# Kernel tuning notes

Measured on AMD Instinct MI355X. Metric: run time of the kernel, lower is better.

The kernel has to match this reference:

```python
import jax, jax.numpy as jnp
import numpy as np

N_NODES = 100000
IN_CH = 128
HID_CH = 128
N_EDGES = 1600000


def setup_inputs() -> dict:
    key = jax.random.key(0)
    ks = jax.random.split(key, 8)
    x = jax.random.normal(ks[0], (N_NODES, IN_CH), dtype=jnp.float32)
    edge_index = jax.random.randint(ks[1], (2, N_EDGES), 0, N_NODES, dtype=jnp.int64)
    s1 = 1.0 / np.sqrt(IN_CH)
    s2 = 1.0 / np.sqrt(HID_CH)
    # SAGEConv layer 1: lin_l (aggregated neighbors, has bias), lin_r (root)
    Wl1 = jax.random.uniform(ks[2], (IN_CH, HID_CH), jnp.float32, -s1, s1)
    Wr1 = jax.random.uniform(ks[3], (IN_CH, HID_CH), jnp.float32, -s1, s1)
    b1 = jnp.zeros((HID_CH,), jnp.float32)
    # SAGEConv layer 2
    Wl2 = jax.random.uniform(ks[4], (HID_CH, HID_CH), jnp.float32, -s2, s2)
    Wr2 = jax.random.uniform(ks[5], (HID_CH, HID_CH), jnp.float32, -s2, s2)
    b2 = jnp.zeros((HID_CH,), jnp.float32)
    return {"x": x, "edge_index": edge_index,
            "Wl1": Wl1, "Wr1": Wr1, "b1": b1,
            "Wl2": Wl2, "Wr2": Wr2, "b2": b2}


def _sage_conv(x, src, dst, inv_deg, Wl, Wr, b):
    # mean aggregation of source-node features into destination nodes
    agg = jax.ops.segment_sum(x[src], dst, num_segments=N_NODES)  # [N, d]
    mean = agg * inv_deg[:, None]
    # out = lin_l(mean_neighbors) + lin_r(x)
    return mean @ Wl + x @ Wr + b


def reference(x, edge_index, Wl1, Wr1, b1, Wl2, Wr2, b2):
    src = edge_index[0]
    dst = edge_index[1]
    deg = jax.ops.segment_sum(jnp.ones_like(dst, dtype=jnp.float32), dst,
                              num_segments=N_NODES)
    inv_deg = 1.0 / jnp.maximum(deg, 1.0)
    h = jax.nn.relu(_sage_conv(x, src, dst, inv_deg, Wl1, Wr1, b1))
    # F.dropout(p=0.2, training=False) is identity in eval mode
    h = jax.nn.relu(_sage_conv(h, src, dst, inv_deg, Wl2, Wr2, b2))
    return h
```

## Files before the change

kernel.cpp:

```cpp
#include <hip/hip_runtime.h>

#define NN 100000
#define NE 1600000
#define CH 128

#define PART 512
#define NP 196
#define PCAP 8704
#define EPB 4096
#define NB 391
#define SCAP 64
#define SLAB 1536

typedef __attribute__((ext_vector_type(8))) short bf16x8;
typedef __attribute__((ext_vector_type(4))) float f32x4;
typedef unsigned int uint;
typedef unsigned short ushort;

__device__ __forceinline__ ushort f2b(float f) {
    uint u = __builtin_bit_cast(uint, f);
    uint r = (u + 0x7fff + ((u >> 16) & 1)) >> 16;
    return (ushort)r;
}
__device__ __forceinline__ float blo(uint v) { return __builtin_bit_cast(float, v << 16); }
__device__ __forceinline__ float bhi(uint v) { return __builtin_bit_cast(float, v & 0xffff0000u); }

__device__ __forceinline__ void acc8(float* a, uint4 v) {
    a[0] += blo(v.x); a[1] += bhi(v.x);
    a[2] += blo(v.y); a[3] += bhi(v.y);
    a[4] += blo(v.z); a[5] += bhi(v.z);
    a[6] += blo(v.w); a[7] += bhi(v.w);
}


__global__ __launch_bounds__(1024) void k_bin(const int4* __restrict__ src4, const int4* __restrict__ dst4,
                                              uint* __restrict__ pcnt, uint* __restrict__ pairbuf) {
    __shared__ uint slots[NP * SCAP];
    __shared__ uint lcnt[NP];
    __shared__ uint lbase[NP];
    int tid = threadIdx.x;
    if (tid < NP) lcnt[tid] = 0;
    __syncthreads();
    int e4 = blockIdx.x * 1024 + tid;
    if (e4 < NE / 4) {
        int4 d4 = dst4[e4];
        int4 s4 = src4[e4];
        int dd[4] = {d4.x, d4.y, d4.z, d4.w};
        int ss[4] = {s4.x, s4.y, s4.z, s4.w};
        #pragma unroll
        for (int j = 0; j < 4; ++j) {
            int p = dd[j] >> 9;
            uint pair = ((uint)(dd[j] & 511) << 17) | (uint)ss[j];
            uint pos = atomicAdd(&lcnt[p], 1u);
            if (pos < SCAP) slots[p * SCAP + pos] = pair;
        }
    }
    __syncthreads();
    if (tid < NP) {
        uint c = lcnt[tid];
        c = c < SCAP ? c : SCAP;
        lcnt[tid] = c;
        lbase[tid] = atomicAdd(&pcnt[tid], c);
    }
    __syncthreads();
    for (int t = tid; t < NP * SCAP; t += 1024) {
        int p = t >> 6;
        uint s = (uint)(t & (SCAP - 1));
        if (s < lcnt[p]) {
            uint idx = lbase[p] + s;
            if (idx < PCAP) pairbuf[(size_t)p * PCAP + idx] = slots[t];
        }
    }
}


__global__ __launch_bounds__(512) void k_csr(const uint* __restrict__ pcnt, const uint* __restrict__ pairbuf,
                                             int* __restrict__ nbrG, uint* __restrict__ pack) {
    __shared__ uint pairs[PCAP];
    __shared__ uint cnt[PART];
    __shared__ uint rowptr[PART + 1];
    __shared__ uint tsum[PART];
    int tid = threadIdx.x;
    int p = blockIdx.x;
    uint tot = pcnt[p];
    tot = tot < PCAP ? tot : PCAP;
    for (uint i = tid; i < tot; i += 512) pairs[i] = pairbuf[(size_t)p * PCAP + i];
    cnt[tid] = 0;
    __syncthreads();
    for (uint i = tid; i < tot; i += 512) atomicAdd(&cnt[pairs[i] >> 17], 1u);
    __syncthreads();
    uint s = cnt[tid];
    tsum[tid] = s;
    __syncthreads();
    for (int off = 1; off < 512; off <<= 1) {
        uint t = (tid >= off) ? tsum[tid - off] : 0;
        __syncthreads();
        tsum[tid] += t;
        __syncthreads();
    }
    rowptr[tid] = tsum[tid] - s;
    if (tid == 511) rowptr[512] = tsum[511];
    __syncthreads();
    cnt[tid] = 0;
    __syncthreads();
    for (uint i = tid; i < tot; i += 512) {
        uint u = pairs[i];
        uint dl = u >> 17;
        uint pos = rowptr[dl] + atomicAdd(&cnt[dl], 1u);
        nbrG[(size_t)p * PCAP + pos] = (int)(u & 0x1FFFFu);
    }
    {
        int n = p * PART + tid;
        if (n < NN) {
            uint deg = rowptr[tid + 1] - rowptr[tid];
            pack[n] = ((uint)(p * PCAP) + rowptr[tid]) | (deg << 21);
        }
    }
}


__global__ __launch_bounds__(256) void k_castx(const float* __restrict__ x, ushort* __restrict__ xb) {
    int n = blockIdx.x * 256 + threadIdx.x;
    int p = blockIdx.y;
    if (n >= NN) return;
    const float4* sp = (const float4*)(x + (size_t)n * 128 + p * 32);
    uint4 o[4];
    ushort* op = (ushort*)o;
    #pragma unroll
    for (int q = 0; q < 8; ++q) {
        float4 v = sp[q];
        op[q * 4 + 0] = f2b(v.x);
        op[q * 4 + 1] = f2b(v.y);
        op[q * 4 + 2] = f2b(v.z);
        op[q * 4 + 3] = f2b(v.w);
    }
    uint4* dp = (uint4*)(xb + ((size_t)p * NN + n) * 32);
    #pragma unroll
    for (int q = 0; q < 4; ++q) dp[q] = o[q];
}

__global__ __launch_bounds__(256) void k_castw(const float* __restrict__ Wl1, const float* __restrict__ Wr1,
                                               const float* __restrict__ Wl2, const float* __restrict__ Wr2,
                                               ushort* __restrict__ BtK1, ushort* __restrict__ BtK2) {
    int i = blockIdx.x * 256 + threadIdx.x;
    const float* Wl = blockIdx.y ? Wl2 : Wl1;
    const float* Wr = blockIdx.y ? Wr2 : Wr1;
    ushort* BtK = blockIdx.y ? BtK2 : BtK1;
    int c = i & 31;
    int n = (i >> 5) & 127;
    int kt = i >> 12;
    int k = kt * 32 + c;
    float v = (k < 128) ? Wl[k * 128 + n] : Wr[(k - 128) * 128 + n];
    BtK[i] = f2b(v);
}


__global__ __launch_bounds__(256) void k_agg(const uint4* __restrict__ feat, const int* __restrict__ nbrG,
                                             const uint* __restrict__ pack, uint4* __restrict__ outb) {
    __shared__ int sl[SLAB];
    __shared__ int sh_s0, sh_cnt;
    int plane = blockIdx.x;
    int nb = blockIdx.y * 64;
    int tid = threadIdx.x;
    int n = nb + (tid >> 2);
    int h = tid & 3;
    if (tid == 0) {
        uint u0 = pack[nb];
        int last = nb + 63 < NN ? nb + 63 : NN - 1;
        uint u1 = pack[last];
        int s0 = (int)(u0 & 0x1FFFFFu);
        sh_s0 = s0;
        sh_cnt = (int)(u1 & 0x1FFFFFu) + (int)(u1 >> 21) - s0;
    }
    __syncthreads();
    int s0 = sh_s0, scnt = sh_cnt;
    bool staged = scnt <= SLAB;
    if (staged) {
        for (int i = tid; i < scnt; i += 256) sl[i] = nbrG[s0 + i];
    }
    __syncthreads();
    if (n >= NN) return;
    uint u = pack[n];
    int s = (int)(u & 0x1FFFFFu);
    int d = (int)(u >> 21);
    const char* fb = (const char*)feat + ((size_t)plane * NN) * 64;
    uint hoff = (uint)h * 16;
    float a[8] = {};
    if (staged) {
        const int* bp = sl + (s - s0);
        int i = 0;
        for (; i + 8 <= d; i += 8) {
            uint off[8];
            uint4 v[8];
            #pragma unroll
            for (int j = 0; j < 8; ++j) off[j] = ((uint)bp[i + j] << 6) | hoff;
            #pragma unroll
            for (int j = 0; j < 8; ++j) v[j] = *(const uint4*)(fb + off[j]);
            #pragma unroll
            for (int j = 0; j < 8; ++j) acc8(a, v[j]);
        }
        for (; i < d; ++i) acc8(a, *(const uint4*)(fb + (((uint)bp[i] << 6) | hoff)));
    } else {
        const int* bp = nbrG + s;
        int i = 0;
        for (; i + 4 <= d; i += 4) {
            uint o0 = ((uint)bp[i] << 6) | hoff;
            uint o1 = ((uint)bp[i + 1] << 6) | hoff;
            uint o2 = ((uint)bp[i + 2] << 6) | hoff;
            uint o3 = ((uint)bp[i + 3] << 6) | hoff;
            uint4 v0 = *(const uint4*)(fb + o0);
            uint4 v1 = *(const uint4*)(fb + o1);
            uint4 v2 = *(const uint4*)(fb + o2);
            uint4 v3 = *(const uint4*)(fb + o3);
            acc8(a, v0);
            acc8(a, v1);
            acc8(a, v2);
            acc8(a, v3);
        }
        for (; i < d; ++i) acc8(a, *(const uint4*)(fb + (((uint)bp[i] << 6) | hoff)));
    }
    float id = 1.0f / fmaxf((float)d, 1.0f);
    uint4 r;
    r.x = (uint)f2b(a[0] * id) | ((uint)f2b(a[1] * id) << 16);
    r.y = (uint)f2b(a[2] * id) | ((uint)f2b(a[3] * id) << 16);
    r.z = (uint)f2b(a[4] * id) | ((uint)f2b(a[5] * id) << 16);
    r.w = (uint)f2b(a[6] * id) | ((uint)f2b(a[7] * id) << 16);
    outb[((size_t)plane * NN + n) * 4 + h] = r;
}


template <bool WB16>
__global__ __launch_bounds__(256) void k_gemm(const ushort* __restrict__ Am, const ushort* Ax,
                                              const ushort* __restrict__ BtK, const float* __restrict__ bias,
                                              void* outp, int M) {
    int lane = threadIdx.x & 63;
    int wave = threadIdx.x >> 6;
    int bm = blockIdx.x * 128 + wave * 32;
    int l16 = lane & 15;
    int lk8 = (lane >> 4) * 8;

    f32x4 acc[2][8] = {};
    #pragma unroll
    for (int kt = 0; kt < 8; ++kt) {
        const ushort* A = (kt < 4) ? Am : Ax;
        int p = kt & 3;
        bf16x8 af[2];
        #pragma unroll
        for (int mt = 0; mt < 2; ++mt) {
            int row = bm + mt * 16 + l16;
            row = row < M ? row : M - 1;
            af[mt] = *(const bf16x8*)(A + ((size_t)p * NN + row) * 32 + lk8);
        }
        const ushort* Bk = BtK + (size_t)kt * 128 * 32;
        #pragma unroll
        for (int nt = 0; nt < 8; ++nt) {
            bf16x8 bfr = *(const bf16x8*)(Bk + (size_t)(nt * 16 + l16) * 32 + lk8);
            acc[0][nt] = __builtin_amdgcn_mfma_f32_16x16x32_bf16(af[0], bfr, acc[0][nt], 0, 0, 0);
            acc[1][nt] = __builtin_amdgcn_mfma_f32_16x16x32_bf16(af[1], bfr, acc[1][nt], 0, 0, 0);
        }
    }
    int mr0 = (lane >> 4) * 4;
    #pragma unroll
    for (int mt = 0; mt < 2; ++mt) {
        #pragma unroll
        for (int r = 0; r < 4; ++r) {
            int m = bm + mt * 16 + mr0 + r;
            if (m < M) {
                #pragma unroll
                for (int nt = 0; nt < 8; ++nt) {
                    float v = acc[mt][nt][r] + bias[nt * 16 + l16];
                    v = v > 0.f ? v : 0.f;
                    if (WB16) {
                        int ch = nt * 16 + l16;
                        ((ushort*)outp)[((size_t)(ch >> 5) * NN + m) * 32 + (ch & 31)] = f2b(v);
                    } else {
                        ((float*)outp)[(size_t)m * 128 + nt * 16 + l16] = v;
                    }
                }
            }
        }
    }
}


static inline size_t alignup(size_t x) { return (x + 255) & ~(size_t)255; }

extern "C" void kernel_launch(void* const* d_in, const int* in_sizes, int n_in,
                              void* d_out, int out_size, void* d_ws, size_t ws_size,
                              hipStream_t stream) {
    const float* x   = (const float*)d_in[0];
    const int* edge  = (const int*)d_in[1];
    const float* Wl1 = (const float*)d_in[2];
    const float* Wr1 = (const float*)d_in[3];
    const float* b1  = (const float*)d_in[4];
    const float* Wl2 = (const float*)d_in[5];
    const float* Wr2 = (const float*)d_in[6];
    const float* b2  = (const float*)d_in[7];
    float* out = (float*)d_out;

    const int* srcp = edge;
    const int* dstp = edge + NE;

    uint* pairbuf = (uint*)d_out;
    int* nbrG = (int*)d_out + (size_t)NP * PCAP;

    char* w = (char*)d_ws;
    uint* pcnt = (uint*)w;     w += alignup((size_t)NP * 4);
    uint* pack = (uint*)w;     w += alignup((size_t)NN * 4);
    ushort* xb = (ushort*)w;   w += alignup((size_t)NN * CH * 2);
    ushort* mb = (ushort*)w;   w += alignup((size_t)NN * CH * 2);
    ushort* BtK1 = (ushort*)w; w += alignup((size_t)128 * 256 * 2);
    ushort* BtK2 = (ushort*)w; w += alignup((size_t)128 * 256 * 2);

    hipMemsetAsync(pcnt, 0, (size_t)NP * 4, stream);

    k_bin<<<NB, 1024, 0, stream>>>((const int4*)srcp, (const int4*)dstp, pcnt, pairbuf);
    k_csr<<<NP, 512, 0, stream>>>(pcnt, pairbuf, nbrG, pack);

    k_castx<<<dim3((NN + 255) / 256, 4), 256, 0, stream>>>(x, xb);
    k_castw<<<dim3(128, 2), 256, 0, stream>>>(Wl1, Wr1, Wl2, Wr2, BtK1, BtK2);

    int gg = (NN + 127) / 128;
    dim3 ag(4, (NN + 63) / 64);
    k_agg<<<ag, 256, 0, stream>>>((const uint4*)xb, nbrG, pack, (uint4*)mb);
    k_gemm<true><<<gg, 256, 0, stream>>>(mb, xb, BtK1, b1, (void*)xb, NN);
    k_agg<<<ag, 256, 0, stream>>>((const uint4*)xb, nbrG, pack, (uint4*)mb);
    k_gemm<false><<<gg, 256, 0, stream>>>(mb, xb, BtK2, b2, (void*)out, NN);
}
```

Baseline: 336.7 us.

## Sort destination nodes by degree within partitions to balance aggregation waves

The CSR build now counting-sorts each partition's 512 destination nodes by in-degree (capped histogram) and lays out rows and pack entries in that sorted order, with an ord array mapping each slot back to its original node id. The aggregation kernel iterates over sorted slots so threads in a wave see similar degrees, which reduces divergence and tail imbalance, and it scatters results to the original node index. The neighbor staging slab is doubled so more 64-node groups fit in shared memory. The costs are extra LDS pressure that may lower occupancy, an extra index load, scattered output writes, and padded slots past the node count that still do gather work before being discarded.

```diff
diff --git a/kernel.cpp b/kernel.cpp
--- a/kernel.cpp
+++ b/kernel.cpp
@@ -10,7 +10,7 @@
 #define EPB 4096
 #define NB 391
 #define SCAP 64
-#define SLAB 1536
+#define SLAB 3072
 
 typedef __attribute__((ext_vector_type(8))) short bf16x8;
 typedef __attribute__((ext_vector_type(4))) float f32x4;
@@ -75,46 +75,60 @@
 
 
 __global__ __launch_bounds__(512) void k_csr(const uint* __restrict__ pcnt, const uint* __restrict__ pairbuf,
-                                             int* __restrict__ nbrG, uint* __restrict__ pack) {
+                                             int* __restrict__ nbrG, uint* __restrict__ pack,
+                                             uint* __restrict__ ord) {
     __shared__ uint pairs[PCAP];
     __shared__ uint cnt[PART];
-    __shared__ uint rowptr[PART + 1];
+    __shared__ uint rankv[PART];
+    __shared__ uint srow[PART + 1];
     __shared__ uint tsum[PART];
+    __shared__ uint hbase[64];
     int tid = threadIdx.x;
     int p = blockIdx.x;
     uint tot = pcnt[p];
     tot = tot < PCAP ? tot : PCAP;
     for (uint i = tid; i < tot; i += 512) pairs[i] = pairbuf[(size_t)p * PCAP + i];
     cnt[tid] = 0;
+    if (tid < 64) hbase[tid] = 0;
     __syncthreads();
     for (uint i = tid; i < tot; i += 512) atomicAdd(&cnt[pairs[i] >> 17], 1u);
     __syncthreads();
-    uint s = cnt[tid];
-    tsum[tid] = s;
-    __syncthreads();
+    uint deg = cnt[tid];
+    uint db = deg < 63 ? deg : 63;
+    atomicAdd(&hbase[db], 1u);
+    __syncthreads();
+    if (tid == 0) {
+        uint s = 0;
+        for (int i = 0; i < 64; ++i) { uint h = hbase[i]; hbase[i] = s; s += h; }
+    }
+    __syncthreads();
+    uint rk = atomicAdd(&hbase[db], 1u);
+    rankv[tid] = rk;
+    tsum[rk] = deg;
+    __syncthreads();
+    uint sd = tsum[tid];
     for (int off = 1; off < 512; off <<= 1) {
         uint t = (tid >= off) ? tsum[tid - off] : 0;
         __syncthreads();
         tsum[tid] += t;
         __syncthreads();
     }
-    rowptr[tid] = tsum[tid] - s;
-    if (tid == 511) rowptr[512] = tsum[511];
+    srow[tid] = tsum[tid] - sd;
+    if (tid == 511) srow[512] = tsum[511];
     __syncthreads();
     cnt[tid] = 0;
     __syncthreads();
     for (uint i = tid; i < tot; i += 512) {
         uint u = pairs[i];
         uint dl = u >> 17;
-        uint pos = rowptr[dl] + atomicAdd(&cnt[dl], 1u);
+        uint pos = srow[rankv[dl]] + atomicAdd(&cnt[dl], 1u);
         nbrG[(size_t)p * PCAP + pos] = (int)(u & 0x1FFFFu);
     }
     {
         int n = p * PART + tid;
-        if (n < NN) {
-            uint deg = rowptr[tid + 1] - rowptr[tid];
-            pack[n] = ((uint)(p * PCAP) + rowptr[tid]) | (deg << 21);
-        }
+        uint q = rankv[tid];
+        pack[(size_t)p * PART + q] = ((uint)(p * PCAP) + srow[q]) | (deg << 21);
+        ord[(size_t)p * PART + q] = (n < NN) ? (uint)n : (uint)NN;
     }
 }
 
@@ -156,7 +170,8 @@
 
 
 __global__ __launch_bounds__(256) void k_agg(const uint4* __restrict__ feat, const int* __restrict__ nbrG,
-                                             const uint* __restrict__ pack, uint4* __restrict__ outb) {
+                                             const uint* __restrict__ pack, const uint* __restrict__ ord,
+                                             uint4* __restrict__ outb) {
     __shared__ int sl[SLAB];
     __shared__ int sh_s0, sh_cnt;
     int plane = blockIdx.x;
@@ -166,8 +181,7 @@
     int h = tid & 3;
     if (tid == 0) {
         uint u0 = pack[nb];
-        int last = nb + 63 < NN ? nb + 63 : NN - 1;
-        uint u1 = pack[last];
+        uint u1 = pack[nb + 63];
         int s0 = (int)(u0 & 0x1FFFFFu);
         sh_s0 = s0;
         sh_cnt = (int)(u1 & 0x1FFFFFu) + (int)(u1 >> 21) - s0;
@@ -179,7 +193,6 @@
         for (int i = tid; i < scnt; i += 256) sl[i] = nbrG[s0 + i];
     }
     __syncthreads();
-    if (n >= NN) return;
     uint u = pack[n];
     int s = (int)(u & 0x1FFFFFu);
     int d = (int)(u >> 21);
@@ -219,13 +232,15 @@
         }
         for (; i < d; ++i) acc8(a, *(const uint4*)(fb + (((uint)bp[i] << 6) | hoff)));
     }
+    int on = (int)ord[n];
+    if (on >= NN) return;
     float id = 1.0f / fmaxf((float)d, 1.0f);
     uint4 r;
     r.x = (uint)f2b(a[0] * id) | ((uint)f2b(a[1] * id) << 16);
     r.y = (uint)f2b(a[2] * id) | ((uint)f2b(a[3] * id) << 16);
     r.z = (uint)f2b(a[4] * id) | ((uint)f2b(a[5] * id) << 16);
     r.w = (uint)f2b(a[6] * id) | ((uint)f2b(a[7] * id) << 16);
-    outb[((size_t)plane * NN + n) * 4 + h] = r;
+    outb[((size_t)plane * NN + on) * 4 + h] = r;
 }
 
 
@@ -306,7 +321,8 @@
 
     char* w = (char*)d_ws;
     uint* pcnt = (uint*)w;     w += alignup((size_t)NP * 4);
-    uint* pack = (uint*)w;     w += alignup((size_t)NN * 4);
+    uint* pack = (uint*)w;     w += alignup((size_t)NP * PART * 4);
+    uint* ordm = (uint*)w;     w += alignup((size_t)NP * PART * 4);
     ushort* xb = (ushort*)w;   w += alignup((size_t)NN * CH * 2);
     ushort* mb = (ushort*)w;   w += alignup((size_t)NN * CH * 2);
     ushort* BtK1 = (ushort*)w; w += alignup((size_t)128 * 256 * 2);
@@ -315,15 +331,15 @@
     hipMemsetAsync(pcnt, 0, (size_t)NP * 4, stream);
 
     k_bin<<<NB, 1024, 0, stream>>>((const int4*)srcp, (const int4*)dstp, pcnt, pairbuf);
-    k_csr<<<NP, 512, 0, stream>>>(pcnt, pairbuf, nbrG, pack);
+    k_csr<<<NP, 512, 0, stream>>>(pcnt, pairbuf, nbrG, pack, ordm);
 
     k_castx<<<dim3((NN + 255) / 256, 4), 256, 0, stream>>>(x, xb);
     k_castw<<<dim3(128, 2), 256, 0, stream>>>(Wl1, Wr1, Wl2, Wr2, BtK1, BtK2);
 
     int gg = (NN + 127) / 128;
-    dim3 ag(4, (NN + 63) / 64);
-    k_agg<<<ag, 256, 0, stream>>>((const uint4*)xb, nbrG, pack, (uint4*)mb);
+    dim3 ag(4, NP * 8);
+    k_agg<<<ag, 256, 0, stream>>>((const uint4*)xb, nbrG, pack, ordm, (uint4*)mb);
     k_gemm<true><<<gg, 256, 0, stream>>>(mb, xb, BtK1, b1, (void*)xb, NN);
-    k_agg<<<ag, 256, 0, stream>>>((const uint4*)xb, nbrG, pack, (uint4*)mb);
+    k_agg<<<ag, 256, 0, stream>>>((const uint4*)xb, nbrG, pack, ordm, (uint4*)mb);
     k_gemm<false><<<gg, 256, 0, stream>>>(mb, xb, BtK2, b2, (void*)out, NN);
 }
```

After: 358.7 us. 6.5% more time.
